# Optimization experiments

Measured on AMD Instinct MI355X. Metric: run time of the kernel, lower is better.

## Reference

```python
import jax, jax.numpy as jnp
import numpy as np

B, S, D, H = 2, 2048, 1024, 16
HD = D // H
SCALE = float(np.sqrt(HD))


def setup_inputs() -> dict:
    key = jax.random.key(0)
    ks = jax.random.split(key, 11)
    mk = lambda k, shape, s=0.02: (jax.random.normal(k, shape, dtype=jnp.float32) * s)
    query = jax.random.normal(ks[0], (B, S, D), dtype=jnp.float32)
    key_t = jax.random.normal(ks[1], (B, S, D), dtype=jnp.float32)
    value = jax.random.normal(ks[2], (B, S, D), dtype=jnp.float32)
    # causal mask: True = position is masked out
    mask = jnp.triu(jnp.ones((S, S), dtype=bool), k=1)
    return {
        "query": query, "key": key_t, "value": value, "mask": mask,
        "Wq": mk(ks[3], (D, D)), "bq": jnp.zeros((D,), jnp.float32),
        "Wk": mk(ks[4], (D, D)), "bk": jnp.zeros((D,), jnp.float32),
        "Wv": mk(ks[5], (D, D)), "bv": jnp.zeros((D,), jnp.float32),
        "Wo": mk(ks[6], (D, D)), "bo": jnp.zeros((D,), jnp.float32),
    }


def reference(query, key, value, mask, Wq, bq, Wk, bk, Wv, bv, Wo, bo):
    b = query.shape[0]
    # projections; nn.Linear computes x @ W.T + b
    q = (query @ Wq.T + bq).reshape(b, -1, H, HD).transpose(0, 2, 1, 3)  # (b,h,sq,hd)
    k = (key @ Wk.T + bk).reshape(b, -1, H, HD).transpose(0, 2, 1, 3)    # (b,h,sk,hd)
    v = (value @ Wv.T + bv).reshape(b, -1, H, HD).transpose(0, 2, 1, 3)  # (b,h,sk,hd)
    scores = jnp.einsum("bhqd,bhkd->bhqk", q, k) / SCALE
    scores = jnp.where(mask[None, None, :, :], -jnp.inf, scores)
    attn_weights = jax.nn.softmax(scores, axis=-1)  # (b,h,sq,sk)
    # dropout is identity in eval mode
    attn_out = jnp.einsum("bhqk,bhkd->bhqd", attn_weights, v)
    attn_out = attn_out.transpose(0, 2, 1, 3).reshape(b, -1, D)
    output = attn_out @ Wo.T + bo
    return output, attn_weights
```

## Files before the change

kernel.cpp:

```cpp
#include <hip/hip_runtime.h>

typedef __bf16 bf16;
typedef __bf16 bf16_8 __attribute__((ext_vector_type(8)));
typedef __bf16 bf16_4 __attribute__((ext_vector_type(4)));
typedef float f32x4 __attribute__((ext_vector_type(4)));

constexpr int kB = 2, kS = 2048, kD = 1024, kH = 16, kHD = 64;
constexpr int kM = kB * kS;
constexpr int kNT = kS / 64;

#define GLOBAL_AS const __attribute__((address_space(1)))
#define LDS_AS __attribute__((address_space(3)))

__device__ __forceinline__ void async_copy16(const bf16* g, bf16* l) {
  __builtin_amdgcn_global_load_lds((GLOBAL_AS unsigned int*)g,
                                   (LDS_AS unsigned int*)l, 16, 0, 0);
}

__device__ __forceinline__ void barrier_lgkm() {
  asm volatile("s_waitcnt lgkmcnt(0)\n\ts_barrier" ::: "memory");
}

__global__ __launch_bounds__(256) void cvt_act(
    const float4* __restrict__ q, const float4* __restrict__ k,
    const float4* __restrict__ v, bf16* __restrict__ oq,
    bf16* __restrict__ ok, bf16* __restrict__ ov) {
  const float4* src = blockIdx.y == 0 ? q : blockIdx.y == 1 ? k : v;
  bf16* dst = blockIdx.y == 0 ? oq : blockIdx.y == 1 ? ok : ov;
  int i = blockIdx.x * 256 + threadIdx.x;
  float4 x = src[i];
  bf16_4 o = {(bf16)x.x, (bf16)x.y, (bf16)x.z, (bf16)x.w};
  *(bf16_4*)(dst + (size_t)i * 4) = o;
}

__global__ __launch_bounds__(256) void cvt_w(
    const float4* __restrict__ a, const float4* __restrict__ b,
    const float4* __restrict__ c, const float4* __restrict__ d,
    bf16* __restrict__ oa, bf16* __restrict__ ob, bf16* __restrict__ oc,
    bf16* __restrict__ od) {
  int z = blockIdx.y;
  const float4* src = z == 0 ? a : z == 1 ? b : z == 2 ? c : d;
  bf16* dst = z == 0 ? oa : z == 1 ? ob : z == 2 ? oc : od;
  int i = blockIdx.x * 256 + threadIdx.x;
  float4 x = src[i];
  bf16_4 o = {(bf16)x.x, (bf16)x.y, (bf16)x.z, (bf16)x.w};
  *(bf16_4*)(dst + (size_t)i * 4) = o;
}

__device__ __forceinline__ void gemm_core(const bf16* __restrict__ A,
                                          const bf16* __restrict__ Bm,
                                          int m0, int n0,
                                          bf16* ldsA, bf16* ldsB,
                                          f32x4 acc[4][4]) {
  const int t = threadIdx.x;
  const int lane = t & 63, wave = t >> 6;
  const int l16 = lane & 15, quad = lane >> 4;
  const int wm = (wave >> 1) * 64, wn = (wave & 1) * 64;
  const f32x4 z4 = {0.f, 0.f, 0.f, 0.f};
#pragma unroll
  for (int i = 0; i < 4; ++i)
#pragma unroll
    for (int j = 0; j < 4; ++j) acc[i][j] = z4;

  for (int kt = 0; kt < kD; kt += 32) {
#pragma unroll
    for (int rep = 0; rep < 2; ++rep) {
      int q = t + rep * 256;
      int row = q >> 2, cc = q & 3;
      bf16* lbase_a = ldsA + (size_t)(wave * 64 + rep * 256) * 8;
      bf16* lbase_b = ldsB + (size_t)(wave * 64 + rep * 256) * 8;
      async_copy16(A + (size_t)(m0 + row) * kD + kt + cc * 8, lbase_a);
      async_copy16(Bm + (size_t)(n0 + row) * kD + kt + cc * 8, lbase_b);
    }
    __syncthreads();
    bf16_8 af[4], bfr[4];
#pragma unroll
    for (int i = 0; i < 4; ++i)
      af[i] = *(const bf16_8*)(ldsA + (wm + i * 16 + l16) * 32 + quad * 8);
#pragma unroll
    for (int j = 0; j < 4; ++j)
      bfr[j] = *(const bf16_8*)(ldsB + (wn + j * 16 + l16) * 32 + quad * 8);
#pragma unroll
    for (int i = 0; i < 4; ++i)
#pragma unroll
      for (int j = 0; j < 4; ++j)
        acc[i][j] = __builtin_amdgcn_mfma_f32_16x16x32_bf16(af[i], bfr[j],
                                                            acc[i][j], 0, 0, 0);
    __syncthreads();
  }
}

__global__ __launch_bounds__(256) void gemm_qkv(
    const bf16* __restrict__ qb, const bf16* __restrict__ kb,
    const bf16* __restrict__ vb, const bf16* __restrict__ wq,
    const bf16* __restrict__ wk, const bf16* __restrict__ wv,
    const float* __restrict__ bq, const float* __restrict__ bk,
    const float* __restrict__ bv, bf16* __restrict__ Qh,
    bf16* __restrict__ Kh, bf16* __restrict__ Vh) {
  __shared__ __align__(16) bf16 ldsA[128 * 32];
  __shared__ __align__(16) bf16 ldsB[128 * 32];
  const bf16 *A, *W;
  const float* bias;
  bf16* Out;
  int z = blockIdx.z;
  if (z == 0) { A = qb; W = wq; bias = bq; Out = Qh; }
  else if (z == 1) { A = kb; W = wk; bias = bk; Out = Kh; }
  else { A = vb; W = wv; bias = bv; Out = Vh; }
  const float scale = (z == 0) ? 0.125f : 1.0f;
  int m0 = blockIdx.x * 128, n0 = blockIdx.y * 128;
  f32x4 acc[4][4];
  gemm_core(A, W, m0, n0, ldsA, ldsB, acc);

  const int t = threadIdx.x, lane = t & 63, wave = t >> 6;
  const int l16 = lane & 15, quad = lane >> 4;
  const int wm = (wave >> 1) * 64, wn = (wave & 1) * 64;
#pragma unroll
  for (int i = 0; i < 4; ++i)
#pragma unroll
    for (int j = 0; j < 4; ++j)
#pragma unroll
      for (int r = 0; r < 4; ++r) {
        int m = m0 + wm + i * 16 + quad * 4 + r;
        int n = n0 + wn + j * 16 + l16;
        float v = (acc[i][j][r] + bias[n]) * scale;
        int b = m >> 11, s = m & (kS - 1);
        int h = n >> 6, hd = n & 63;
        Out[((size_t)(b * kH + h) * kS + s) * kHD + hd] = (bf16)v;
      }
}

__global__ __launch_bounds__(256) void transpose_v(const bf16* __restrict__ Vh,
                                                   bf16* __restrict__ Vt) {
  __shared__ bf16 tile[64][72];
  const int t = threadIdx.x;
  const int s0 = blockIdx.x * 64, bh = blockIdx.y;
#pragma unroll
  for (int it = 0; it < 2; ++it) {
    int chunk = t + it * 256;
    int s = chunk >> 3, d0 = (chunk & 7) * 8;
    bf16_8 v = *(const bf16_8*)(Vh + ((size_t)bh * kS + s0 + s) * kHD + d0);
#pragma unroll
    for (int j = 0; j < 8; ++j) tile[d0 + j][s] = v[j];
  }
  __syncthreads();
#pragma unroll
  for (int it = 0; it < 2; ++it) {
    int chunk = t + it * 256;
    int d = chunk >> 3, c0 = (chunk & 7) * 8;
    bf16_8 o = *(const bf16_8*)&tile[d][c0];
    *(bf16_8*)(Vt + ((size_t)bh * kHD + d) * kS + s0 + c0) = o;
  }
}

__global__ __launch_bounds__(256) void gemm_out(const bf16* __restrict__ AO,
                                                const bf16* __restrict__ wo,
                                                const float* __restrict__ bo,
                                                float* __restrict__ Cout) {
  __shared__ __align__(16) bf16 ldsA[128 * 32];
  __shared__ __align__(16) bf16 ldsB[128 * 32];
  int m0 = blockIdx.x * 128, n0 = blockIdx.y * 128;
  f32x4 acc[4][4];
  gemm_core(AO, wo, m0, n0, ldsA, ldsB, acc);

  const int t = threadIdx.x, lane = t & 63, wave = t >> 6;
  const int l16 = lane & 15, quad = lane >> 4;
  const int wm = (wave >> 1) * 64, wn = (wave & 1) * 64;
#pragma unroll
  for (int i = 0; i < 4; ++i)
#pragma unroll
    for (int j = 0; j < 4; ++j)
#pragma unroll
      for (int r = 0; r < 4; ++r) {
        int m = m0 + wm + i * 16 + quad * 4 + r;
        int n = n0 + wn + j * 16 + l16;
        Cout[(size_t)m * kD + n] = acc[i][j][r] + bo[n];
      }
}

__global__ __launch_bounds__(256) void attn_kernel(
    const bf16* __restrict__ Qh, const bf16* __restrict__ Kh,
    const bf16* __restrict__ Vt, float* __restrict__ attnW,
    bf16* __restrict__ AO) {
  __shared__ __align__(16) bf16 ldsK[2][64 * 64];
  __shared__ __align__(16) bf16 ldsV[2][64 * 64];
  __shared__ __align__(16) bf16 ldsP[64 * 64];

  const int t = threadIdx.x, lane = t & 63, wave = t >> 6;
  const int l16 = lane & 15, quad = lane >> 4;
  const int bh = blockIdx.x;
  const int qt = (kNT - 1) - blockIdx.y;
  const int q0 = qt * 64;

  const bf16* Qbase = Qh + ((size_t)bh * kS + q0) * kHD;
  const bf16* Kbase = Kh + (size_t)bh * kS * kHD;
  const bf16* Vtbase = Vt + (size_t)bh * kHD * kS;

  bf16_8 aq0 = *(const bf16_8*)(Qbase + (wave * 16 + l16) * kHD + quad * 8);
  bf16_8 aq1 = *(const bf16_8*)(Qbase + (wave * 16 + l16) * kHD + 32 + quad * 8);

  const int dq = t >> 3, dc = (t & 7) * 8;
#define ISSUE_K(kt, buf)                                                      \
  {                                                                           \
    const int k0_ = (kt) * 64;                                                \
    async_copy16(Kbase + (size_t)(k0_ / 64 * 64 + dq) * kHD + dc,             \
                 &ldsK[buf][(size_t)(wave * 64) * 8]);                        \
    async_copy16(Kbase + (size_t)(k0_ + ((t + 256) >> 3)) * kHD +             \
                     (((t + 256) & 7) * 8),                                   \
                 &ldsK[buf][(size_t)(wave * 64 + 256) * 8]);                  \
  }
#define ISSUE_V(kt, buf)                                                      \
  {                                                                           \
    const int k0_ = (kt) * 64;                                                \
    async_copy16(Vtbase + (size_t)dq * kS + k0_ + dc,                         \
                 &ldsV[buf][(size_t)(wave * 64) * 8]);                        \
    async_copy16(Vtbase + (size_t)((t + 256) >> 3) * kS + k0_ +               \
                     (((t + 256) & 7) * 8),                                   \
                 &ldsV[buf][(size_t)(wave * 64 + 256) * 8]);                  \
  }

  float lp[4] = {0.f, 0.f, 0.f, 0.f};
  {
    const int k0f = 0;
    async_copy16(Kbase + (size_t)(k0f + dq) * kHD + dc,
                 &ldsK[0][(size_t)(wave * 64) * 8]);
    async_copy16(Kbase + (size_t)(k0f + ((t + 256) >> 3)) * kHD +
                     (((t + 256) & 7) * 8),
                 &ldsK[0][(size_t)(wave * 64 + 256) * 8]);
  }
  for (int kt = 0; kt <= qt; ++kt) {
    __syncthreads();
    if (kt < qt) ISSUE_K(kt + 1, (kt + 1) & 1);
    const bf16* Kl = ldsK[kt & 1];
    const int k0 = kt * 64;
    f32x4 sacc[4];
#pragma unroll
    for (int j = 0; j < 4; ++j) {
      bf16_8 b0 = *(const bf16_8*)(Kl + (j * 16 + l16) * 64 + quad * 8);
      bf16_8 b1 = *(const bf16_8*)(Kl + (j * 16 + l16) * 64 + 32 + quad * 8);
      f32x4 z = {0.f, 0.f, 0.f, 0.f};
      z = __builtin_amdgcn_mfma_f32_16x16x32_bf16(aq0, b0, z, 0, 0, 0);
      z = __builtin_amdgcn_mfma_f32_16x16x32_bf16(aq1, b1, z, 0, 0, 0);
      sacc[j] = z;
    }
#pragma unroll
    for (int j = 0; j < 4; ++j)
#pragma unroll
      for (int r = 0; r < 4; ++r) {
        int qrow = q0 + wave * 16 + quad * 4 + r;
        int kcol = k0 + j * 16 + l16;
        lp[r] += (kcol > qrow) ? 0.f : __expf(sacc[j][r]);
      }
  }
  float rl[4];
#pragma unroll
  for (int r = 0; r < 4; ++r) {
    float s = lp[r];
#pragma unroll
    for (int off = 1; off < 16; off <<= 1) s += __shfl_xor(s, off, 64);
    rl[r] = 1.0f / s;
  }

  const f32x4 z4 = {0.f, 0.f, 0.f, 0.f};
  f32x4 oacc[4];
#pragma unroll
  for (int d = 0; d < 4; ++d) oacc[d] = z4;

  __syncthreads();
  ISSUE_K(0, 0);
  ISSUE_V(0, 0);
  for (int kt = 0; kt <= qt; ++kt) {
    __syncthreads();
    if (kt < qt) {
      ISSUE_K(kt + 1, (kt + 1) & 1);
      ISSUE_V(kt + 1, (kt + 1) & 1);
    }
    const bf16* Kl = ldsK[kt & 1];
    const bf16* Vl = ldsV[kt & 1];
    const int k0 = kt * 64;
    f32x4 sacc[4];
#pragma unroll
    for (int j = 0; j < 4; ++j) {
      bf16_8 b0 = *(const bf16_8*)(Kl + (j * 16 + l16) * 64 + quad * 8);
      bf16_8 b1 = *(const bf16_8*)(Kl + (j * 16 + l16) * 64 + 32 + quad * 8);
      f32x4 z = {0.f, 0.f, 0.f, 0.f};
      z = __builtin_amdgcn_mfma_f32_16x16x32_bf16(aq0, b0, z, 0, 0, 0);
      z = __builtin_amdgcn_mfma_f32_16x16x32_bf16(aq1, b1, z, 0, 0, 0);
      sacc[j] = z;
    }
#pragma unroll
    for (int j = 0; j < 4; ++j)
#pragma unroll
      for (int r = 0; r < 4; ++r) {
        int qrl = wave * 16 + quad * 4 + r;
        int qrow = q0 + qrl;
        int kcol = k0 + j * 16 + l16;
        float p = (kcol > qrow) ? 0.f : __expf(sacc[j][r]) * rl[r];
        attnW[((size_t)bh * kS + qrow) * kS + kcol] = p;
        ldsP[(size_t)qrl * 64 + j * 16 + l16] = (bf16)p;
      }
    barrier_lgkm();
    bf16_8 ap0 = *(const bf16_8*)(ldsP + (wave * 16 + l16) * 64 + quad * 8);
    bf16_8 ap1 = *(const bf16_8*)(ldsP + (wave * 16 + l16) * 64 + 32 + quad * 8);
#pragma unroll
    for (int dsub = 0; dsub < 4; ++dsub) {
      bf16_8 bv0 = *(const bf16_8*)(Vl + (dsub * 16 + l16) * 64 + quad * 8);
      bf16_8 bv1 = *(const bf16_8*)(Vl + (dsub * 16 + l16) * 64 + 32 + quad * 8);
      oacc[dsub] = __builtin_amdgcn_mfma_f32_16x16x32_bf16(ap0, bv0, oacc[dsub], 0, 0, 0);
      oacc[dsub] = __builtin_amdgcn_mfma_f32_16x16x32_bf16(ap1, bv1, oacc[dsub], 0, 0, 0);
    }
  }
  for (int kt = qt + 1; kt < kNT; ++kt) {
    const float4 zf = {0.f, 0.f, 0.f, 0.f};
    int row = t >> 2;
    float* dst = attnW + ((size_t)bh * kS + q0 + row) * kS + kt * 64 + (t & 3) * 16;
#pragma unroll
    for (int f = 0; f < 4; ++f) ((float4*)dst)[f] = zf;
  }

  const int b = bh >> 4, h = bh & 15;
#pragma unroll
  for (int dsub = 0; dsub < 4; ++dsub)
#pragma unroll
    for (int r = 0; r < 4; ++r) {
      int qrow = q0 + wave * 16 + quad * 4 + r;
      int d = dsub * 16 + l16;
      AO[((size_t)(b * kS + qrow)) * kD + h * kHD + d] = (bf16)oacc[dsub][r];
    }
#undef ISSUE_K
#undef ISSUE_V
}

extern "C" void kernel_launch(void* const* d_in, const int* in_sizes, int n_in,
                              void* d_out, int out_size, void* d_ws, size_t ws_size,
                              hipStream_t stream) {
  const float* query = (const float*)d_in[0];
  const float* key_t = (const float*)d_in[1];
  const float* value = (const float*)d_in[2];
  const float* Wq = (const float*)d_in[4];
  const float* bq = (const float*)d_in[5];
  const float* Wk = (const float*)d_in[6];
  const float* bk = (const float*)d_in[7];
  const float* Wv = (const float*)d_in[8];
  const float* bv = (const float*)d_in[9];
  const float* Wo = (const float*)d_in[10];
  const float* bo = (const float*)d_in[11];

  float* out = (float*)d_out;
  float* attnW = out + (size_t)kM * kD;

  bf16* qb = (bf16*)d_ws;
  bf16* kb = qb + (size_t)kM * kD;
  bf16* vb = kb + (size_t)kM * kD;
  bf16* Qh = vb + (size_t)kM * kD;
  bf16* Kh = Qh + (size_t)kM * kD;
  bf16* Vh = Kh + (size_t)kM * kD;
  bf16* Vtr = Vh + (size_t)kM * kD;
  bf16* AO = Vtr + (size_t)kM * kD;
  bf16* wqb = AO + (size_t)kM * kD;
  bf16* wkb = wqb + (size_t)kD * kD;
  bf16* wvb = wkb + (size_t)kD * kD;
  bf16* wob = wvb + (size_t)kD * kD;

  const int n4_x = kM * kD / 4;
  const int n4_w = kD * kD / 4;
  cvt_act<<<dim3(n4_x / 256, 3), 256, 0, stream>>>(
      (const float4*)query, (const float4*)key_t, (const float4*)value,
      qb, kb, vb);
  cvt_w<<<dim3(n4_w / 256, 4), 256, 0, stream>>>(
      (const float4*)Wq, (const float4*)Wk, (const float4*)Wv,
      (const float4*)Wo, wqb, wkb, wvb, wob);

  gemm_qkv<<<dim3(kM / 128, kD / 128, 3), 256, 0, stream>>>(
      qb, kb, vb, wqb, wkb, wvb, bq, bk, bv, Qh, Kh, Vh);

  transpose_v<<<dim3(kS / 64, kB * kH), 256, 0, stream>>>(Vh, Vtr);

  attn_kernel<<<dim3(kB * kH, kNT), 256, 0, stream>>>(Qh, Kh, Vtr, attnW, AO);

  gemm_out<<<dim3(kM / 128, kD / 128), 256, 0, stream>>>(AO, wob, bo, out);
}
```

Measured before the change: 765.3 us.

## Restructure attention passes, coalesce attn weight stores, shrink output GEMM tile

The first softmax pass now processes 128-key tiles and applies the causal mask only on the last tile. The second pass writes attention weights through an LDS strip, so each lane stores contiguous float4 rows instead of scattered scalars. LDS is merged into a single buffer, and the unneeded lgkm wait before reading P is dropped. The output GEMM uses 64x128 tiles with its own inline loop to double the block count. This also makes attnW values round-trip through bf16, which loses precision in the returned weights.

New measurement: 797.0 us. 1.04x slower.

```diff
diff --git a/kernel.cpp b/kernel.cpp
--- a/kernel.cpp
+++ b/kernel.cpp
@@ -15,10 +15,6 @@
 __device__ __forceinline__ void async_copy16(const bf16* g, bf16* l) {
   __builtin_amdgcn_global_load_lds((GLOBAL_AS unsigned int*)g,
                                    (LDS_AS unsigned int*)l, 16, 0, 0);
-}
-
-__device__ __forceinline__ void barrier_lgkm() {
-  asm volatile("s_waitcnt lgkmcnt(0)\n\ts_barrier" ::: "memory");
 }
 
 __global__ __launch_bounds__(256) void cvt_act(
@@ -156,17 +152,47 @@
                                                 const bf16* __restrict__ wo,
                                                 const float* __restrict__ bo,
                                                 float* __restrict__ Cout) {
-  __shared__ __align__(16) bf16 ldsA[128 * 32];
+  __shared__ __align__(16) bf16 ldsA[64 * 32];
   __shared__ __align__(16) bf16 ldsB[128 * 32];
-  int m0 = blockIdx.x * 128, n0 = blockIdx.y * 128;
-  f32x4 acc[4][4];
-  gemm_core(AO, wo, m0, n0, ldsA, ldsB, acc);
-
   const int t = threadIdx.x, lane = t & 63, wave = t >> 6;
   const int l16 = lane & 15, quad = lane >> 4;
-  const int wm = (wave >> 1) * 64, wn = (wave & 1) * 64;
-#pragma unroll
-  for (int i = 0; i < 4; ++i)
+  const int wm = (wave >> 1) * 32, wn = (wave & 1) * 64;
+  const int m0 = blockIdx.x * 64, n0 = blockIdx.y * 128;
+  const f32x4 z4 = {0.f, 0.f, 0.f, 0.f};
+  f32x4 acc[2][4];
+#pragma unroll
+  for (int i = 0; i < 2; ++i)
+#pragma unroll
+    for (int j = 0; j < 4; ++j) acc[i][j] = z4;
+
+  for (int kt = 0; kt < kD; kt += 32) {
+    async_copy16(AO + (size_t)(m0 + (t >> 2)) * kD + kt + (t & 3) * 8,
+                 ldsA + (size_t)(wave * 64) * 8);
+    async_copy16(wo + (size_t)(n0 + (t >> 2)) * kD + kt + (t & 3) * 8,
+                 ldsB + (size_t)(wave * 64) * 8);
+    {
+      int c = t + 256;
+      async_copy16(wo + (size_t)(n0 + (c >> 2)) * kD + kt + (c & 3) * 8,
+                   ldsB + (size_t)(wave * 64 + 256) * 8);
+    }
+    __syncthreads();
+    bf16_8 af[2], bfr[4];
+#pragma unroll
+    for (int i = 0; i < 2; ++i)
+      af[i] = *(const bf16_8*)(ldsA + (wm + i * 16 + l16) * 32 + quad * 8);
+#pragma unroll
+    for (int j = 0; j < 4; ++j)
+      bfr[j] = *(const bf16_8*)(ldsB + (wn + j * 16 + l16) * 32 + quad * 8);
+#pragma unroll
+    for (int i = 0; i < 2; ++i)
+#pragma unroll
+      for (int j = 0; j < 4; ++j)
+        acc[i][j] = __builtin_amdgcn_mfma_f32_16x16x32_bf16(af[i], bfr[j],
+                                                            acc[i][j], 0, 0, 0);
+    __syncthreads();
+  }
+#pragma unroll
+  for (int i = 0; i < 2; ++i)
 #pragma unroll
     for (int j = 0; j < 4; ++j)
 #pragma unroll
@@ -181,9 +207,8 @@
     const bf16* __restrict__ Qh, const bf16* __restrict__ Kh,
     const bf16* __restrict__ Vt, float* __restrict__ attnW,
     bf16* __restrict__ AO) {
-  __shared__ __align__(16) bf16 ldsK[2][64 * 64];
-  __shared__ __align__(16) bf16 ldsV[2][64 * 64];
-  __shared__ __align__(16) bf16 ldsP[64 * 64];
+  __shared__ __align__(16) bf16 smem[20480];
+  bf16* const Pstrip = smem + 16384;
 
   const int t = threadIdx.x, lane = t & 63, wave = t >> 6;
   const int l16 = lane & 15, quad = lane >> 4;
@@ -198,40 +223,90 @@
   bf16_8 aq0 = *(const bf16_8*)(Qbase + (wave * 16 + l16) * kHD + quad * 8);
   bf16_8 aq1 = *(const bf16_8*)(Qbase + (wave * 16 + l16) * kHD + 32 + quad * 8);
 
-  const int dq = t >> 3, dc = (t & 7) * 8;
-#define ISSUE_K(kt, buf)                                                      \
-  {                                                                           \
-    const int k0_ = (kt) * 64;                                                \
-    async_copy16(Kbase + (size_t)(k0_ / 64 * 64 + dq) * kHD + dc,             \
-                 &ldsK[buf][(size_t)(wave * 64) * 8]);                        \
-    async_copy16(Kbase + (size_t)(k0_ + ((t + 256) >> 3)) * kHD +             \
-                     (((t + 256) & 7) * 8),                                   \
-                 &ldsK[buf][(size_t)(wave * 64 + 256) * 8]);                  \
-  }
-#define ISSUE_V(kt, buf)                                                      \
-  {                                                                           \
-    const int k0_ = (kt) * 64;                                                \
-    async_copy16(Vtbase + (size_t)dq * kS + k0_ + dc,                         \
-                 &ldsV[buf][(size_t)(wave * 64) * 8]);                        \
-    async_copy16(Vtbase + (size_t)((t + 256) >> 3) * kS + k0_ +               \
-                     (((t + 256) & 7) * 8),                                   \
-                 &ldsV[buf][(size_t)(wave * 64 + 256) * 8]);                  \
+#define ISSUE_BIG(bt, buf)                                                   \
+  {                                                                          \
+    _Pragma("unroll") for (int rep = 0; rep < 4; ++rep) {                    \
+      int c = t + rep * 256;                                                 \
+      async_copy16(Kbase + (size_t)((bt)*128 + (c >> 3)) * kHD + (c & 7) * 8,\
+                   smem + (buf)*8192 + (size_t)(wave * 64 + rep * 256) * 8); \
+    }                                                                        \
+  }
+#define ISSUE_K2(kt, buf)                                                    \
+  {                                                                          \
+    _Pragma("unroll") for (int rep = 0; rep < 2; ++rep) {                    \
+      int c = t + rep * 256;                                                 \
+      async_copy16(Kbase + (size_t)((kt)*64 + (c >> 3)) * kHD + (c & 7) * 8, \
+                   smem + (buf)*8192 + (size_t)(wave * 64 + rep * 256) * 8); \
+    }                                                                        \
+  }
+#define ISSUE_V2(kt, buf)                                                    \
+  {                                                                          \
+    _Pragma("unroll") for (int rep = 0; rep < 2; ++rep) {                    \
+      int c = t + rep * 256;                                                 \
+      async_copy16(Vtbase + (size_t)(c >> 3) * kS + (kt)*64 + (c & 7) * 8,   \
+                   smem + (buf)*8192 + 4096 +                                \
+                       (size_t)(wave * 64 + rep * 256) * 8);                 \
+    }                                                                        \
   }
 
   float lp[4] = {0.f, 0.f, 0.f, 0.f};
-  {
-    const int k0f = 0;
-    async_copy16(Kbase + (size_t)(k0f + dq) * kHD + dc,
-                 &ldsK[0][(size_t)(wave * 64) * 8]);
-    async_copy16(Kbase + (size_t)(k0f + ((t + 256) >> 3)) * kHD +
-                     (((t + 256) & 7) * 8),
-                 &ldsK[0][(size_t)(wave * 64 + 256) * 8]);
-  }
+  const int nbig = (qt + 2) >> 1;
+  ISSUE_BIG(0, 0);
+  for (int bt = 0; bt < nbig; ++bt) {
+    __syncthreads();
+    if (bt + 1 < nbig) ISSUE_BIG(bt + 1, (bt + 1) & 1);
+    const bf16* Kl = smem + (bt & 1) * 8192;
+    f32x4 sacc[8];
+#pragma unroll
+    for (int j = 0; j < 8; ++j) {
+      bf16_8 b0 = *(const bf16_8*)(Kl + (j * 16 + l16) * 64 + quad * 8);
+      bf16_8 b1 = *(const bf16_8*)(Kl + (j * 16 + l16) * 64 + 32 + quad * 8);
+      f32x4 z = {0.f, 0.f, 0.f, 0.f};
+      z = __builtin_amdgcn_mfma_f32_16x16x32_bf16(aq0, b0, z, 0, 0, 0);
+      z = __builtin_amdgcn_mfma_f32_16x16x32_bf16(aq1, b1, z, 0, 0, 0);
+      sacc[j] = z;
+    }
+    if (bt == nbig - 1) {
+#pragma unroll
+      for (int j = 0; j < 8; ++j)
+#pragma unroll
+        for (int r = 0; r < 4; ++r) {
+          int qrow = q0 + wave * 16 + quad * 4 + r;
+          int kcol = bt * 128 + j * 16 + l16;
+          lp[r] += (kcol > qrow) ? 0.f : __expf(sacc[j][r]);
+        }
+    } else {
+#pragma unroll
+      for (int j = 0; j < 8; ++j)
+#pragma unroll
+        for (int r = 0; r < 4; ++r) lp[r] += __expf(sacc[j][r]);
+    }
+  }
+  __syncthreads();
+  ISSUE_K2(0, 0);
+  ISSUE_V2(0, 0);
+  float rl[4];
+#pragma unroll
+  for (int r = 0; r < 4; ++r) {
+    float s = lp[r];
+#pragma unroll
+    for (int off = 1; off < 16; off <<= 1) s += __shfl_xor(s, off, 64);
+    rl[r] = 1.0f / s;
+  }
+
+  const f32x4 z4 = {0.f, 0.f, 0.f, 0.f};
+  f32x4 oacc[4];
+#pragma unroll
+  for (int d = 0; d < 4; ++d) oacc[d] = z4;
+
   for (int kt = 0; kt <= qt; ++kt) {
     __syncthreads();
-    if (kt < qt) ISSUE_K(kt + 1, (kt + 1) & 1);
-    const bf16* Kl = ldsK[kt & 1];
-    const int k0 = kt * 64;
+    if (kt < qt) {
+      ISSUE_K2(kt + 1, (kt + 1) & 1);
+      ISSUE_V2(kt + 1, (kt + 1) & 1);
+    }
+    const bf16* Kl = smem + (kt & 1) * 8192;
+    const bf16* Vl = Kl + 4096;
     f32x4 sacc[4];
 #pragma unroll
     for (int j = 0; j < 4; ++j) {
@@ -242,65 +317,45 @@
       z = __builtin_amdgcn_mfma_f32_16x16x32_bf16(aq1, b1, z, 0, 0, 0);
       sacc[j] = z;
     }
-#pragma unroll
-    for (int j = 0; j < 4; ++j)
-#pragma unroll
-      for (int r = 0; r < 4; ++r) {
-        int qrow = q0 + wave * 16 + quad * 4 + r;
-        int kcol = k0 + j * 16 + l16;
-        lp[r] += (kcol > qrow) ? 0.f : __expf(sacc[j][r]);
-      }
-  }
-  float rl[4];
-#pragma unroll
-  for (int r = 0; r < 4; ++r) {
-    float s = lp[r];
-#pragma unroll
-    for (int off = 1; off < 16; off <<= 1) s += __shfl_xor(s, off, 64);
-    rl[r] = 1.0f / s;
-  }
-
-  const f32x4 z4 = {0.f, 0.f, 0.f, 0.f};
-  f32x4 oacc[4];
-#pragma unroll
-  for (int d = 0; d < 4; ++d) oacc[d] = z4;
-
-  __syncthreads();
-  ISSUE_K(0, 0);
-  ISSUE_V(0, 0);
-  for (int kt = 0; kt <= qt; ++kt) {
-    __syncthreads();
-    if (kt < qt) {
-      ISSUE_K(kt + 1, (kt + 1) & 1);
-      ISSUE_V(kt + 1, (kt + 1) & 1);
-    }
-    const bf16* Kl = ldsK[kt & 1];
-    const bf16* Vl = ldsV[kt & 1];
-    const int k0 = kt * 64;
-    f32x4 sacc[4];
-#pragma unroll
-    for (int j = 0; j < 4; ++j) {
-      bf16_8 b0 = *(const bf16_8*)(Kl + (j * 16 + l16) * 64 + quad * 8);
-      bf16_8 b1 = *(const bf16_8*)(Kl + (j * 16 + l16) * 64 + 32 + quad * 8);
-      f32x4 z = {0.f, 0.f, 0.f, 0.f};
-      z = __builtin_amdgcn_mfma_f32_16x16x32_bf16(aq0, b0, z, 0, 0, 0);
-      z = __builtin_amdgcn_mfma_f32_16x16x32_bf16(aq1, b1, z, 0, 0, 0);
-      sacc[j] = z;
-    }
-#pragma unroll
-    for (int j = 0; j < 4; ++j)
-#pragma unroll
-      for (int r = 0; r < 4; ++r) {
-        int qrl = wave * 16 + quad * 4 + r;
-        int qrow = q0 + qrl;
-        int kcol = k0 + j * 16 + l16;
-        float p = (kcol > qrow) ? 0.f : __expf(sacc[j][r]) * rl[r];
-        attnW[((size_t)bh * kS + qrow) * kS + kcol] = p;
-        ldsP[(size_t)qrl * 64 + j * 16 + l16] = (bf16)p;
-      }
-    barrier_lgkm();
-    bf16_8 ap0 = *(const bf16_8*)(ldsP + (wave * 16 + l16) * 64 + quad * 8);
-    bf16_8 ap1 = *(const bf16_8*)(ldsP + (wave * 16 + l16) * 64 + 32 + quad * 8);
+    if (kt == qt) {
+#pragma unroll
+      for (int j = 0; j < 4; ++j)
+#pragma unroll
+        for (int r = 0; r < 4; ++r) {
+          int qrl = wave * 16 + quad * 4 + r;
+          int kcol = kt * 64 + j * 16 + l16;
+          float p = __expf(sacc[j][r]) * rl[r];
+          if (kcol > q0 + qrl) p = 0.f;
+          Pstrip[(size_t)qrl * 64 + j * 16 + l16] = (bf16)p;
+        }
+    } else {
+#pragma unroll
+      for (int j = 0; j < 4; ++j)
+#pragma unroll
+        for (int r = 0; r < 4; ++r) {
+          int qrl = wave * 16 + quad * 4 + r;
+          float p = __expf(sacc[j][r]) * rl[r];
+          Pstrip[(size_t)qrl * 64 + j * 16 + l16] = (bf16)p;
+        }
+    }
+    {
+      int row = lane >> 2, c0 = (lane & 3) * 16;
+      const bf16* src = Pstrip + (size_t)(wave * 16 + row) * 64 + c0;
+      bf16_8 pa = *(const bf16_8*)src;
+      bf16_8 pb = *(const bf16_8*)(src + 8);
+      float* dst =
+          attnW + ((size_t)bh * kS + q0 + wave * 16 + row) * kS + kt * 64 + c0;
+      float4 f0 = {(float)pa[0], (float)pa[1], (float)pa[2], (float)pa[3]};
+      float4 f1 = {(float)pa[4], (float)pa[5], (float)pa[6], (float)pa[7]};
+      float4 f2 = {(float)pb[0], (float)pb[1], (float)pb[2], (float)pb[3]};
+      float4 f3 = {(float)pb[4], (float)pb[5], (float)pb[6], (float)pb[7]};
+      ((float4*)dst)[0] = f0;
+      ((float4*)dst)[1] = f1;
+      ((float4*)dst)[2] = f2;
+      ((float4*)dst)[3] = f3;
+    }
+    bf16_8 ap0 = *(const bf16_8*)(Pstrip + (size_t)(wave * 16 + l16) * 64 + quad * 8);
+    bf16_8 ap1 = *(const bf16_8*)(Pstrip + (size_t)(wave * 16 + l16) * 64 + 32 + quad * 8);
 #pragma unroll
     for (int dsub = 0; dsub < 4; ++dsub) {
       bf16_8 bv0 = *(const bf16_8*)(Vl + (dsub * 16 + l16) * 64 + quad * 8);
@@ -309,6 +364,7 @@
       oacc[dsub] = __builtin_amdgcn_mfma_f32_16x16x32_bf16(ap1, bv1, oacc[dsub], 0, 0, 0);
     }
   }
+
   for (int kt = qt + 1; kt < kNT; ++kt) {
     const float4 zf = {0.f, 0.f, 0.f, 0.f};
     int row = t >> 2;
@@ -326,8 +382,9 @@
       int d = dsub * 16 + l16;
       AO[((size_t)(b * kS + qrow)) * kD + h * kHD + d] = (bf16)oacc[dsub][r];
     }
-#undef ISSUE_K
-#undef ISSUE_V
+#undef ISSUE_BIG
+#undef ISSUE_K2
+#undef ISSUE_V2
 }
 
 extern "C" void kernel_launch(void* const* d_in, const int* in_sizes, int n_in,
@@ -377,5 +434,5 @@
 
   attn_kernel<<<dim3(kB * kH, kNT), 256, 0, stream>>>(Qh, Kh, Vtr, attnW, AO);
 
-  gemm_out<<<dim3(kM / 128, kD / 128), 256, 0, stream>>>(AO, wob, bo, out);
-}
+  gemm_out<<<dim3(kM / 64, kD / 128), 256, 0, stream>>>(AO, wob, bo, out);
+}
```
